# Kernel optimization log

Hardware: AMD Instinct MI355X
Metric: run time of the kernel (lower is better)

The kernel has to match this reference:

```python
import jax, jax.numpy as jnp
import numpy as np

MAX_ITER = 20
F_TOL = 1e-6
FREE_NUM = 64  # free_idx[1] + 1
TRUNC = (0, 512)  # truncate_idx


def setup_inputs() -> dict:
    key = jax.random.key(0)
    ks = jax.random.split(key, 8)
    bsz, in_dim, hid, out_dim, m = 1024, 512, 1024, 256, 128
    return {
        "b_primal": jax.random.normal(ks[0], (bsz, in_dim), jnp.float32),
        "W0": jax.random.normal(ks[1], (hid, in_dim), jnp.float32) / np.sqrt(in_dim).astype(np.float32),
        "b0": jnp.zeros((hid,), jnp.float32),
        "W1": jax.random.normal(ks[2], (hid, hid), jnp.float32) / np.sqrt(hid).astype(np.float32),
        "b1": jnp.zeros((hid,), jnp.float32),
        "W2": jax.random.normal(ks[3], (out_dim, hid), jnp.float32) / np.sqrt(hid).astype(np.float32),
        "b2": jnp.zeros((out_dim,), jnp.float32),
        "A": jax.random.normal(ks[4], (m, out_dim), jnp.float32) * 0.1,
        "b_vec": jax.random.normal(ks[5], (m,), jnp.float32),
        # scaled so spectral norm < 1 -> contracting fixed-point iteration
        "WzProj": jax.random.normal(ks[6], (out_dim, out_dim), jnp.float32) * 0.03,
        "WbProj": jax.random.normal(ks[7], (out_dim, m), jnp.float32) * 0.1,
    }


def reference(b_primal, W0, b0, W1, b1, W2, b2, A, b_vec, WzProj, WbProj):
    # eval-mode forward of DualNN (report_projection=True)
    x = b_primal[:, TRUNC[0]:TRUNC[1]]
    h = jax.nn.relu(x @ W0.T + b0)
    h = jax.nn.relu(h @ W1.T + b1)
    out = h @ W2.T + b2                      # [bsz, output_dim]

    bias_proj = b_vec @ WbProj.T             # [output_dim]

    def cond(state):
        _, it, res = state
        return (it <= MAX_ITER) & (res > F_TOL)

    def body(state):
        z, it, _ = state
        z = bias_proj + z @ WzProj.T         # affine projection step
        u = z[:, :FREE_NUM]
        v = jax.nn.relu(z[:, FREE_NUM:])     # clamp non-free coordinates
        z = jnp.concatenate([u, v], axis=-1)
        res = jnp.max(jnp.abs(z @ A.T - b_vec))  # inf-norm equality residual
        return z, it + 1, res

    z_star, curr_iter, _ = jax.lax.while_loop(
        cond, body, (out, jnp.int32(1), jnp.float32(jnp.inf)))
    return (z_star, out, curr_iter)
```

## Files before the change

### kernel.cpp

```cpp
#include <hip/hip_runtime.h>

typedef __attribute__((ext_vector_type(8))) __bf16 bf16x8;
typedef __attribute__((ext_vector_type(4))) float f32x4;

#define MAX_ITER_N 20
#define F_TOL_F 1e-6f
#define FREE_NUM_N 64

#define BSZ 1024
#define IN_DIM 512
#define HID 1024
#define OUT_DIM 256
#define M_CON 128

#define WS_DONE  0
#define WS_RES   8
#define WS_BP    48
#define WS_H1    304
#define WS_H2    (WS_H1 + 524288)
#define WS_W2C   (WS_H2 + 524288)
#define WS_WZG   (WS_W2C + 131072)
#define WS_AG    (WS_WZG + 32768)

__device__ __forceinline__ unsigned short f2bf(float f) {
    unsigned int u = __float_as_uint(f);
    u += 0x7fffu + ((u >> 16) & 1u);
    return (unsigned short)(u >> 16);
}

__device__ __forceinline__ unsigned int pk2(float a, float b) {
    return (unsigned int)f2bf(a) | ((unsigned int)f2bf(b) << 16);
}

__device__ __forceinline__ void cvt16(const float* s, unsigned short* d) {
    float4 v0 = *(const float4*)s,       v1 = *(const float4*)(s + 4),
           v2 = *(const float4*)(s + 8), v3 = *(const float4*)(s + 12);
    *(uint4*)d       = (uint4){pk2(v0.x, v0.y), pk2(v0.z, v0.w), pk2(v1.x, v1.y), pk2(v1.z, v1.w)};
    *(uint4*)(d + 8) = (uint4){pk2(v2.x, v2.y), pk2(v2.z, v2.w), pk2(v3.x, v3.y), pk2(v3.z, v3.w)};
}

__device__ __forceinline__ void gload_lds16(const unsigned short* g, unsigned short* l) {
    __builtin_amdgcn_global_load_lds(
        (const __attribute__((address_space(1))) unsigned int*)(const void*)g,
        (__attribute__((address_space(3))) unsigned int*)(void*)l, 16, 0, 0);
}

__device__ __forceinline__ bf16x8 frag128(const unsigned short* lds, int row, int gc) {
    int phys = gc ^ (row & 15);
    return __builtin_bit_cast(bf16x8, *(const uint4*)(lds + row * 128 + phys * 8));
}

template<int K, bool AF32, bool RELU>
__global__ __launch_bounds__(256) void gemm_k(
    const void* __restrict__ Ap, const float* __restrict__ Bf,
    const float* __restrict__ bias, unsigned short* __restrict__ C,
    float* __restrict__ ws,
    const float* __restrict__ W2, const float* __restrict__ Wz,
    const float* __restrict__ Am, const float* __restrict__ b_vec,
    const float* __restrict__ WbP)
{
    constexpr int NCH = K / 128;
    __shared__ __align__(16) unsigned short sA[2][8192];
    __shared__ __align__(16) unsigned short sB[2][8192];

    const int tid = threadIdx.x;

    if constexpr (AF32) {
        if (blockIdx.x >= 256) {
            int eb = blockIdx.x - 256;
            unsigned short* W2c = (unsigned short*)(ws + WS_W2C);
            unsigned short* WzG = (unsigned short*)(ws + WS_WZG);
            unsigned short* AG  = (unsigned short*)(ws + WS_AG);
            float* bp = ws + WS_BP;
            if (eb < 64) {
                int base = eb * 4096 + tid * 16;
                cvt16(W2 + base, W2c + base);
            } else if (eb < 80) {
                int base = (eb - 64) * 4096 + tid * 16;
                cvt16(Wz + base, WzG + base);
            } else if (eb < 88) {
                int base = (eb - 80) * 4096 + tid * 16;
                cvt16(Am + base, AG + base);
            } else {
                if (eb == 88 && tid < 48) ((unsigned int*)ws)[tid] = 0u;
                int j  = (eb - 88) * 32 + (tid >> 3);
                int kg = tid & 7;
                const float* p = WbP + j * M_CON + kg * 16;
                float s = 0.0f;
#pragma unroll
                for (int i = 0; i < 16; ++i) s += p[i] * b_vec[kg * 16 + i];
#pragma unroll
                for (int off = 4; off > 0; off >>= 1) s += __shfl_xor(s, off);
                if (kg == 0) bp[j] = s;
            }
            return;
        }
    }

    const int w = tid >> 6;
    const int lane = tid & 63;
    const int ln = lane & 15;
    const int q  = lane >> 4;
    const int wr = w >> 1;
    const int wc = w & 1;
    const int row0 = (blockIdx.x >> 4) * 64;
    const int col0 = (blockIdx.x & 15) * 64;

    int grow[4], ggc[4], lof[4];
#pragma unroll
    for (int i = 0; i < 4; ++i) {
        int P = tid + 256 * i;
        grow[i] = P >> 4; ggc[i] = P & 15;
        lof[i] = grow[i] * 128 + (ggc[i] ^ (grow[i] & 15)) * 8;
    }
    int soff[4], dbase[4];
    const unsigned short* Ab_h = (const unsigned short*)Ap + row0 * K;
    const float*          Ab_f = (const float*)Ap + row0 * K;
    if constexpr (!AF32) {
#pragma unroll
        for (int i = 0; i < 4; ++i) {
            int P = w * 256 + i * 64 + lane;
            int row = P >> 4, pgc = P & 15;
            soff[i]  = row * K + (pgc ^ (row & 15)) * 8;
            dbase[i] = (w * 256 + i * 64) * 8;
        }
    }
    const float* Bb = Bf + col0 * K;

    float4 ra[8], rb[8];

    if constexpr (AF32) {
#pragma unroll
        for (int i = 0; i < 4; ++i) {
            const float* s = Ab_f + grow[i] * K + ggc[i] * 8;
            ra[2*i]   = *(const float4*)s;
            ra[2*i+1] = *(const float4*)(s + 4);
        }
    } else {
#pragma unroll
        for (int i = 0; i < 4; ++i) gload_lds16(Ab_h + soff[i], &sA[0][dbase[i]]);
    }
#pragma unroll
    for (int i = 0; i < 4; ++i) {
        const float* s = Bb + grow[i] * K + ggc[i] * 8;
        rb[2*i]   = *(const float4*)s;
        rb[2*i+1] = *(const float4*)(s + 4);
    }
    if constexpr (AF32) {
#pragma unroll
        for (int i = 0; i < 4; ++i)
            *(uint4*)(&sA[0][lof[i]]) = (uint4){
                pk2(ra[2*i].x, ra[2*i].y),   pk2(ra[2*i].z, ra[2*i].w),
                pk2(ra[2*i+1].x, ra[2*i+1].y), pk2(ra[2*i+1].z, ra[2*i+1].w)};
    }
#pragma unroll
    for (int i = 0; i < 4; ++i)
        *(uint4*)(&sB[0][lof[i]]) = (uint4){
            pk2(rb[2*i].x, rb[2*i].y),   pk2(rb[2*i].z, rb[2*i].w),
            pk2(rb[2*i+1].x, rb[2*i+1].y), pk2(rb[2*i+1].z, rb[2*i+1].w)};

    f32x4 acc[2][2];
#pragma unroll
    for (int rm = 0; rm < 2; ++rm)
#pragma unroll
        for (int cn = 0; cn < 2; ++cn)
            acc[rm][cn] = (f32x4){0.f, 0.f, 0.f, 0.f};

    for (int c = 0; c < NCH; ++c) {
        __syncthreads();
        const int nb = (c + 1) & 1;
        if (c + 1 < NCH) {
            const int koff = (c + 1) * 128;
            if constexpr (AF32) {
#pragma unroll
                for (int i = 0; i < 4; ++i) {
                    const float* s = Ab_f + grow[i] * K + koff + ggc[i] * 8;
                    ra[2*i]   = *(const float4*)s;
                    ra[2*i+1] = *(const float4*)(s + 4);
                }
            } else {
#pragma unroll
                for (int i = 0; i < 4; ++i)
                    gload_lds16(Ab_h + koff + soff[i], &sA[nb][dbase[i]]);
            }
#pragma unroll
            for (int i = 0; i < 4; ++i) {
                const float* s = Bb + grow[i] * K + koff + ggc[i] * 8;
                rb[2*i]   = *(const float4*)s;
                rb[2*i+1] = *(const float4*)(s + 4);
            }
        }
        const unsigned short* Ac = sA[c & 1];
        const unsigned short* Bc = sB[c & 1];
#pragma unroll
        for (int ks = 0; ks < 4; ++ks) {
            bf16x8 af0 = frag128(Ac, wr * 32 + ln,      ks * 4 + q);
            bf16x8 af1 = frag128(Ac, wr * 32 + 16 + ln, ks * 4 + q);
            bf16x8 bf0 = frag128(Bc, wc * 32 + ln,      ks * 4 + q);
            bf16x8 bf1 = frag128(Bc, wc * 32 + 16 + ln, ks * 4 + q);
            acc[0][0] = __builtin_amdgcn_mfma_f32_16x16x32_bf16(af0, bf0, acc[0][0], 0, 0, 0);
            acc[0][1] = __builtin_amdgcn_mfma_f32_16x16x32_bf16(af0, bf1, acc[0][1], 0, 0, 0);
            acc[1][0] = __builtin_amdgcn_mfma_f32_16x16x32_bf16(af1, bf0, acc[1][0], 0, 0, 0);
            acc[1][1] = __builtin_amdgcn_mfma_f32_16x16x32_bf16(af1, bf1, acc[1][1], 0, 0, 0);
        }
        if (c + 1 < NCH) {
            if constexpr (AF32) {
#pragma unroll
                for (int i = 0; i < 4; ++i)
                    *(uint4*)(&sA[nb][lof[i]]) = (uint4){
                        pk2(ra[2*i].x, ra[2*i].y),   pk2(ra[2*i].z, ra[2*i].w),
                        pk2(ra[2*i+1].x, ra[2*i+1].y), pk2(ra[2*i+1].z, ra[2*i+1].w)};
            }
#pragma unroll
            for (int i = 0; i < 4; ++i)
                *(uint4*)(&sB[nb][lof[i]]) = (uint4){
                    pk2(rb[2*i].x, rb[2*i].y),   pk2(rb[2*i].z, rb[2*i].w),
                    pk2(rb[2*i+1].x, rb[2*i+1].y), pk2(rb[2*i+1].z, rb[2*i+1].w)};
        }
    }

#pragma unroll
    for (int cn = 0; cn < 2; ++cn) {
        const int cc = col0 + wc * 32 + cn * 16 + ln;
        const float bv = bias[cc];
#pragma unroll
        for (int rm = 0; rm < 2; ++rm)
#pragma unroll
            for (int i = 0; i < 4; ++i) {
                int r = row0 + wr * 32 + rm * 16 + q * 4 + i;
                float v = acc[rm][cn][i] + bv;
                if (RELU) v = fmaxf(v, 0.0f);
                C[r * HID + cc] = f2bf(v);
            }
    }
}

__global__ __launch_bounds__(512, 1) void k3_k(
    const float* __restrict__ b2v, const float* __restrict__ b_vec,
    const float* __restrict__ Wzf, float* __restrict__ out,
    float* __restrict__ ws)
{
    __shared__ __align__(16) unsigned short hS[16 * 1024];
    __shared__ __align__(16) unsigned short zS[2][16][264];
    __shared__ float redL[MAX_ITER_N * 8];
    __shared__ float Tsh;
    __shared__ int hotI;

    unsigned int* done = (unsigned int*)ws;
    unsigned int* res  = (unsigned int*)(ws + WS_RES);
    const float* bp = ws + WS_BP;
    const unsigned short* h2c = (const unsigned short*)(ws + WS_H2);
    const unsigned short* W2c = (const unsigned short*)(ws + WS_W2C);
    const unsigned short* WzG = (const unsigned short*)(ws + WS_WZG);
    const unsigned short* AG  = (const unsigned short*)(ws + WS_AG);
    float* outz = out + BSZ * OUT_DIM;

    const int tid  = threadIdx.x;
    const int wave = tid >> 6;
    const int lane = tid & 63;
    const int ln   = lane & 15;
    const int q    = lane >> 4;
    const int bid  = blockIdx.x;
    const int r0   = bid * 16;

#pragma unroll
    for (int i = 0; i < 4; ++i) {
        int G = wave * 256 + i * 64 + lane;
        int row = G >> 7, phys = G & 127;
        int gc = (phys & ~15) | ((phys & 15) ^ (row & 15));
        gload_lds16(h2c + (r0 + row) * HID + gc * 8, &hS[(wave * 256 + i * 64) * 8]);
    }

    int colg[2];
    colg[0] = wave * 32 + ln;
    colg[1] = wave * 32 + 16 + ln;
    const bool relu0 = (wave * 32) >= FREE_NUM_N;
    const bool relu1 = (wave * 32 + 16) >= FREE_NUM_N;

    bf16x8 afr[8];
    const int m = wave * 16 + ln;
    const float bvv = b_vec[m];
#pragma unroll
    for (int ks = 0; ks < 8; ++ks)
        afr[ks] = __builtin_bit_cast(bf16x8, *(const uint4*)(AG + m * OUT_DIM + ks * 32 + q * 8));
    float bpv[2];
    bf16x8 wzfr[2][8];
#pragma unroll
    for (int nt = 0; nt < 2; ++nt) {
        bpv[nt] = bp[colg[nt]];
#pragma unroll
        for (int ks = 0; ks < 8; ++ks)
            wzfr[nt][ks] = __builtin_bit_cast(bf16x8, *(const uint4*)(WzG + colg[nt] * OUT_DIM + ks * 32 + q * 8));
    }
    __syncthreads();

    const f32x4 zero4 = {0.f, 0.f, 0.f, 0.f};

    f32x4 a3a[2], a3b[2];
    a3a[0] = zero4; a3a[1] = zero4; a3b[0] = zero4; a3b[1] = zero4;
#pragma unroll 4
    for (int ks = 0; ks < 16; ++ks) {
        int gciA = ks * 4 + q;
        int physA = (gciA & ~15) | ((gciA & 15) ^ ln);
        bf16x8 afA = __builtin_bit_cast(bf16x8, *(const uint4*)&hS[ln * 1024 + physA * 8]);
        int gciB = (ks + 16) * 4 + q;
        int physB = (gciB & ~15) | ((gciB & 15) ^ ln);
        bf16x8 afB = __builtin_bit_cast(bf16x8, *(const uint4*)&hS[ln * 1024 + physB * 8]);
#pragma unroll
        for (int nt = 0; nt < 2; ++nt) {
            bf16x8 wfA = __builtin_bit_cast(bf16x8, *(const uint4*)(W2c + colg[nt] * HID + ks * 32 + q * 8));
            bf16x8 wfB = __builtin_bit_cast(bf16x8, *(const uint4*)(W2c + colg[nt] * HID + (ks + 16) * 32 + q * 8));
            a3a[nt] = __builtin_amdgcn_mfma_f32_16x16x32_bf16(afA, wfA, a3a[nt], 0, 0, 0);
            a3b[nt] = __builtin_amdgcn_mfma_f32_16x16x32_bf16(afB, wfB, a3b[nt], 0, 0, 0);
        }
    }

#pragma unroll
    for (int nt = 0; nt < 2; ++nt) {
        float bv = b2v[colg[nt]];
#pragma unroll
        for (int i = 0; i < 4; ++i) {
            float v = a3a[nt][i] + a3b[nt][i] + bv;
            outz[(r0 + q * 4 + i) * OUT_DIM + colg[nt]] = v;
            zS[0][q * 4 + i][colg[nt]] = f2bf(v);
        }
    }
    __syncthreads();

    bf16x8 zfr[8];
#pragma unroll
    for (int ks = 0; ks < 8; ++ks)
        zfr[ks] = __builtin_bit_cast(bf16x8, *(const uint4*)&zS[0][ln][ks * 32 + q * 8]);

    int wb = 1;

    for (int t = 1; t <= MAX_ITER_N; ++t) {
        f32x4 aA[2], aB[2], r2a, r2b;
        aA[0] = zero4; aA[1] = zero4; aB[0] = zero4; aB[1] = zero4;
        r2a = zero4; r2b = zero4;
#pragma unroll
        for (int ks = 0; ks < 4; ++ks) {
#pragma unroll
            for (int nt = 0; nt < 2; ++nt) {
                aA[nt] = __builtin_amdgcn_mfma_f32_16x16x32_bf16(zfr[ks],     wzfr[nt][ks],     aA[nt], 0, 0, 0);
                aB[nt] = __builtin_amdgcn_mfma_f32_16x16x32_bf16(zfr[ks + 4], wzfr[nt][ks + 4], aB[nt], 0, 0, 0);
            }
            if (t > 1) {
                r2a = __builtin_amdgcn_mfma_f32_16x16x32_bf16(zfr[ks],     afr[ks],     r2a, 0, 0, 0);
                r2b = __builtin_amdgcn_mfma_f32_16x16x32_bf16(zfr[ks + 4], afr[ks + 4], r2b, 0, 0, 0);
            }
        }
        float vals[2][4];
#pragma unroll
        for (int nt = 0; nt < 2; ++nt) {
            const bool rl = nt ? relu1 : relu0;
#pragma unroll
            for (int i = 0; i < 4; ++i) {
                float v = aA[nt][i] + aB[nt][i] + bpv[nt];
                if (rl) v = fmaxf(v, 0.0f);
                vals[nt][i] = v;
            }
        }
        if (t > 1) {
            float lmax = 0.0f;
#pragma unroll
            for (int i = 0; i < 4; ++i)
                lmax = fmaxf(lmax, fabsf(r2a[i] + r2b[i] - bvv));
#pragma unroll
            for (int off = 32; off > 0; off >>= 1)
                lmax = fmaxf(lmax, __shfl_xor(lmax, off));
            if (lane == 0) redL[(t - 2) * 8 + wave] = lmax;
        }
        if (t == MAX_ITER_N) {
#pragma unroll
            for (int nt = 0; nt < 2; ++nt)
#pragma unroll
                for (int i = 0; i < 4; ++i)
                    out[(r0 + q * 4 + i) * OUT_DIM + colg[nt]] = vals[nt][i];
        }
#pragma unroll
        for (int nt = 0; nt < 2; ++nt)
#pragma unroll
            for (int i = 0; i < 4; ++i)
                zS[wb][q * 4 + i][colg[nt]] = f2bf(vals[nt][i]);
        __syncthreads();
#pragma unroll
        for (int ks = 0; ks < 8; ++ks)
            zfr[ks] = __builtin_bit_cast(bf16x8, *(const uint4*)&zS[wb][ln][ks * 32 + q * 8]);
        wb ^= 1;
    }

    {
        f32x4 r2a = zero4, r2b = zero4;
#pragma unroll
        for (int ks = 0; ks < 4; ++ks) {
            r2a = __builtin_amdgcn_mfma_f32_16x16x32_bf16(zfr[ks],     afr[ks],     r2a, 0, 0, 0);
            r2b = __builtin_amdgcn_mfma_f32_16x16x32_bf16(zfr[ks + 4], afr[ks + 4], r2b, 0, 0, 0);
        }
        float lmax = 0.0f;
#pragma unroll
        for (int i = 0; i < 4; ++i)
            lmax = fmaxf(lmax, fabsf(r2a[i] + r2b[i] - bvv));
#pragma unroll
        for (int off = 32; off > 0; off >>= 1)
            lmax = fmaxf(lmax, __shfl_xor(lmax, off));
        if (lane == 0) redL[19 * 8 + wave] = lmax;
    }
    __syncthreads();

    bool lhot = true;
    if (tid < MAX_ITER_N) {
        float rv = redL[tid * 8];
#pragma unroll
        for (int w2 = 1; w2 < 8; ++w2) rv = fmaxf(rv, redL[tid * 8 + w2]);
        atomicMax(res + tid, __float_as_uint(rv));
        lhot = (rv > F_TOL_F);
    }
    if (tid < 64) {
        unsigned long long mm = __ballot((tid < MAX_ITER_N) && lhot);
        if (tid == 0) hotI = ((mm & 0xFFFFFull) == 0xFFFFFull) ? 1 : 0;
    }
    __syncthreads();

    if (tid == 0) {
        __threadfence();
        atomicAdd(done, 1u);
    }

    if (hotI) {
        if (bid == 0 && tid == 0)
            out[2 * BSZ * OUT_DIM] = (float)(MAX_ITER_N + 1);
        return;
    }

    if (tid == 0) {
        while (__hip_atomic_load(done, __ATOMIC_ACQUIRE, __HIP_MEMORY_SCOPE_AGENT) < 64u)
            __builtin_amdgcn_s_sleep(2);
    }
    __syncthreads();

    {
        float rv = 1e30f;
        if (tid < MAX_ITER_N)
            rv = __uint_as_float(__hip_atomic_load(res + tid, __ATOMIC_ACQUIRE, __HIP_MEMORY_SCOPE_AGENT));
        if (tid < 64) {
            unsigned long long mm = __ballot((tid < MAX_ITER_N) && !(rv > F_TOL_F));
            if (tid == 0) Tsh = (float)(mm ? (int)__ffsll(mm) : MAX_ITER_N);
        }
        __syncthreads();
    }
    const int T = (int)Tsh;
    if (bid == 0 && tid == 0)
        out[2 * BSZ * OUT_DIM] = (float)(T + 1);
    if (T >= MAX_ITER_N) return;

    {
        float (*zF)[257] = (float(*)[257])hS;
        const int row = tid >> 4;
        const int c0 = (tid & 15) * 16;
        if (tid < 256)
            for (int i = 0; i < 16; ++i)
                zF[row][c0 + i] = outz[(r0 + row) * OUT_DIM + c0 + i];
        __syncthreads();
        const int j = tid;
        const float bj = (tid < 256) ? bp[j] : 0.0f;
        for (int t = 0; t < T; ++t) {
            float acc[16] = {};
            if (tid < 256) {
                for (int k = 0; k < OUT_DIM; ++k) {
                    float wv = Wzf[j * OUT_DIM + k];
#pragma unroll
                    for (int r = 0; r < 16; ++r) acc[r] += zF[r][k] * wv;
                }
            }
            __syncthreads();
            if (tid < 256) {
#pragma unroll
                for (int r = 0; r < 16; ++r) {
                    float v = acc[r] + bj;
                    if (j >= FREE_NUM_N) v = fmaxf(v, 0.0f);
                    zF[r][j] = v;
                }
            }
            __syncthreads();
        }
        if (tid < 256)
            for (int i = 0; i < 16; ++i)
                out[(r0 + row) * OUT_DIM + c0 + i] = zF[row][c0 + i];
    }
}

extern "C" void kernel_launch(void* const* d_in, const int* in_sizes, int n_in,
                              void* d_out, int out_size, void* d_ws, size_t ws_size,
                              hipStream_t stream) {
    const float* b_primal = (const float*)d_in[0];
    const float* W0     = (const float*)d_in[1];
    const float* b0     = (const float*)d_in[2];
    const float* W1     = (const float*)d_in[3];
    const float* b1     = (const float*)d_in[4];
    const float* W2     = (const float*)d_in[5];
    const float* b2     = (const float*)d_in[6];
    const float* Amat   = (const float*)d_in[7];
    const float* b_vec  = (const float*)d_in[8];
    const float* WzProj = (const float*)d_in[9];
    const float* WbProj = (const float*)d_in[10];
    float* out = (float*)d_out;
    float* ws  = (float*)d_ws;

    unsigned short* h1c = (unsigned short*)(ws + WS_H1);
    unsigned short* h2c = (unsigned short*)(ws + WS_H2);

    hipLaunchKernelGGL((gemm_k<IN_DIM, true, true>), dim3(352), dim3(256), 0, stream,
                       (const void*)b_primal, W0, b0, h1c, ws,
                       W2, WzProj, Amat, b_vec, WbProj);
    hipLaunchKernelGGL((gemm_k<HID, false, true>), dim3(256), dim3(256), 0, stream,
                       (const void*)h1c, W1, b1, h2c, ws,
                       nullptr, nullptr, nullptr, nullptr, nullptr);
    hipLaunchKernelGGL(k3_k, dim3(64), dim3(512), 0, stream,
                       b2, b_vec, WzProj, out, ws);
}
```

Before: 137.6 us.

## Fuse second hidden-layer GEMM into fixed-point kernel and drop separate launch

Removes the standalone layer-2 GEMM launch and computes relu(h1 @ W1.T + b1) per 16-row block inside the final kernel, writing the result into a new swizzled LDS buffer that feeds the W2 GEMM. W1 is converted to bf16 by extra blocks in the first kernel, reusing the old h2 workspace region. This saves a launch and the h2 global round trip, but runs the largest GEMM on only 64 blocks, each streaming all of W1 from global memory, which risks lower parallelism and higher L2 traffic.

```diff
diff --git a/kernel.cpp b/kernel.cpp
--- a/kernel.cpp
+++ b/kernel.cpp
@@ -57,7 +57,7 @@
     float* __restrict__ ws,
     const float* __restrict__ W2, const float* __restrict__ Wz,
     const float* __restrict__ Am, const float* __restrict__ b_vec,
-    const float* __restrict__ WbP)
+    const float* __restrict__ WbP, const float* __restrict__ W1f)
 {
     constexpr int NCH = K / 128;
     __shared__ __align__(16) unsigned short sA[2][8192];
@@ -71,6 +71,7 @@
             unsigned short* W2c = (unsigned short*)(ws + WS_W2C);
             unsigned short* WzG = (unsigned short*)(ws + WS_WZG);
             unsigned short* AG  = (unsigned short*)(ws + WS_AG);
+            unsigned short* W1c = (unsigned short*)(ws + WS_H2);
             float* bp = ws + WS_BP;
             if (eb < 64) {
                 int base = eb * 4096 + tid * 16;
@@ -81,7 +82,7 @@
             } else if (eb < 88) {
                 int base = (eb - 80) * 4096 + tid * 16;
                 cvt16(Am + base, AG + base);
-            } else {
+            } else if (eb < 96) {
                 if (eb == 88 && tid < 48) ((unsigned int*)ws)[tid] = 0u;
                 int j  = (eb - 88) * 32 + (tid >> 3);
                 int kg = tid & 7;
@@ -92,6 +93,9 @@
 #pragma unroll
                 for (int off = 4; off > 0; off >>= 1) s += __shfl_xor(s, off);
                 if (kg == 0) bp[j] = s;
+            } else {
+                int base = (eb - 96) * 4096 + tid * 16;
+                cvt16(W1f + base, W1c + base);
             }
             return;
         }
@@ -236,11 +240,12 @@
 }
 
 __global__ __launch_bounds__(512, 1) void k3_k(
-    const float* __restrict__ b2v, const float* __restrict__ b_vec,
-    const float* __restrict__ Wzf, float* __restrict__ out,
-    float* __restrict__ ws)
+    const float* __restrict__ b1f, const float* __restrict__ b2v,
+    const float* __restrict__ b_vec, const float* __restrict__ Wzf,
+    float* __restrict__ out, float* __restrict__ ws)
 {
-    __shared__ __align__(16) unsigned short hS[16 * 1024];
+    __shared__ __align__(16) unsigned short hS1[16 * 1024];
+    __shared__ __align__(16) unsigned short hS2[16 * 1024];
     __shared__ __align__(16) unsigned short zS[2][16][264];
     __shared__ float redL[MAX_ITER_N * 8];
     __shared__ float Tsh;
@@ -249,7 +254,8 @@
     unsigned int* done = (unsigned int*)ws;
     unsigned int* res  = (unsigned int*)(ws + WS_RES);
     const float* bp = ws + WS_BP;
-    const unsigned short* h2c = (const unsigned short*)(ws + WS_H2);
+    const unsigned short* h1c = (const unsigned short*)(ws + WS_H1);
+    const unsigned short* W1c = (const unsigned short*)(ws + WS_H2);
     const unsigned short* W2c = (const unsigned short*)(ws + WS_W2C);
     const unsigned short* WzG = (const unsigned short*)(ws + WS_WZG);
     const unsigned short* AG  = (const unsigned short*)(ws + WS_AG);
@@ -268,7 +274,7 @@
         int G = wave * 256 + i * 64 + lane;
         int row = G >> 7, phys = G & 127;
         int gc = (phys & ~15) | ((phys & 15) ^ (row & 15));
-        gload_lds16(h2c + (r0 + row) * HID + gc * 8, &hS[(wave * 256 + i * 64) * 8]);
+        gload_lds16(h1c + (r0 + row) * HID + gc * 8, &hS1[(wave * 256 + i * 64) * 8]);
     }
 
     int colg[2];
@@ -292,9 +298,43 @@
         for (int ks = 0; ks < 8; ++ks)
             wzfr[nt][ks] = __builtin_bit_cast(bf16x8, *(const uint4*)(WzG + colg[nt] * OUT_DIM + ks * 32 + q * 8));
     }
+    float b1t[8];
+#pragma unroll
+    for (int ct = 0; ct < 8; ++ct) b1t[ct] = b1f[wave * 128 + ct * 16 + ln];
     __syncthreads();
 
     const f32x4 zero4 = {0.f, 0.f, 0.f, 0.f};
+
+    {
+        f32x4 hacc[8];
+#pragma unroll
+        for (int ct = 0; ct < 8; ++ct) hacc[ct] = zero4;
+#pragma unroll 2
+        for (int ks = 0; ks < 32; ++ks) {
+            int gci = ks * 4 + q;
+            int phys = (gci & ~15) | ((gci & 15) ^ ln);
+            bf16x8 af = __builtin_bit_cast(bf16x8, *(const uint4*)&hS1[ln * 1024 + phys * 8]);
+#pragma unroll
+            for (int ct = 0; ct < 8; ++ct) {
+                bf16x8 wf = __builtin_bit_cast(bf16x8,
+                    *(const uint4*)(W1c + (wave * 128 + ct * 16 + ln) * HID + ks * 32 + q * 8));
+                hacc[ct] = __builtin_amdgcn_mfma_f32_16x16x32_bf16(af, wf, hacc[ct], 0, 0, 0);
+            }
+        }
+#pragma unroll
+        for (int ct = 0; ct < 8; ++ct) {
+            const int c = wave * 128 + ct * 16 + ln;
+            const int g = c >> 3;
+#pragma unroll
+            for (int i = 0; i < 4; ++i) {
+                float v = fmaxf(hacc[ct][i] + b1t[ct], 0.0f);
+                int row = q * 4 + i;
+                int pg = (g & ~15) | ((g & 15) ^ (row & 15));
+                hS2[row * 1024 + pg * 8 + (c & 7)] = f2bf(v);
+            }
+        }
+    }
+    __syncthreads();
 
     f32x4 a3a[2], a3b[2];
     a3a[0] = zero4; a3a[1] = zero4; a3b[0] = zero4; a3b[1] = zero4;
@@ -302,10 +342,10 @@
     for (int ks = 0; ks < 16; ++ks) {
         int gciA = ks * 4 + q;
         int physA = (gciA & ~15) | ((gciA & 15) ^ ln);
-        bf16x8 afA = __builtin_bit_cast(bf16x8, *(const uint4*)&hS[ln * 1024 + physA * 8]);
+        bf16x8 afA = __builtin_bit_cast(bf16x8, *(const uint4*)&hS2[ln * 1024 + physA * 8]);
         int gciB = (ks + 16) * 4 + q;
         int physB = (gciB & ~15) | ((gciB & 15) ^ ln);
-        bf16x8 afB = __builtin_bit_cast(bf16x8, *(const uint4*)&hS[ln * 1024 + physB * 8]);
+        bf16x8 afB = __builtin_bit_cast(bf16x8, *(const uint4*)&hS2[ln * 1024 + physB * 8]);
 #pragma unroll
         for (int nt = 0; nt < 2; ++nt) {
             bf16x8 wfA = __builtin_bit_cast(bf16x8, *(const uint4*)(W2c + colg[nt] * HID + ks * 32 + q * 8));
@@ -455,7 +495,7 @@
     if (T >= MAX_ITER_N) return;
 
     {
-        float (*zF)[257] = (float(*)[257])hS;
+        float (*zF)[257] = (float(*)[257])hS1;
         const int row = tid >> 4;
         const int c0 = (tid & 15) * 16;
         if (tid < 256)
@@ -508,14 +548,10 @@
     float* ws  = (float*)d_ws;
 
     unsigned short* h1c = (unsigned short*)(ws + WS_H1);
-    unsigned short* h2c = (unsigned short*)(ws + WS_H2);
-
-    hipLaunchKernelGGL((gemm_k<IN_DIM, true, true>), dim3(352), dim3(256), 0, stream,
+
+    hipLaunchKernelGGL((gemm_k<IN_DIM, true, true>), dim3(608), dim3(256), 0, stream,
                        (const void*)b_primal, W0, b0, h1c, ws,
-                       W2, WzProj, Amat, b_vec, WbProj);
-    hipLaunchKernelGGL((gemm_k<HID, false, true>), dim3(256), dim3(256), 0, stream,
-                       (const void*)h1c, W1, b1, h2c, ws,
-                       nullptr, nullptr, nullptr, nullptr, nullptr);
+                       W2, WzProj, Amat, b_vec, WbProj, W1);
     hipLaunchKernelGGL(k3_k, dim3(64), dim3(512), 0, stream,
-                       b2, b_vec, WzProj, out, ws);
-}
+                       b1, b2, b_vec, WzProj, out, ws);
+}
```

After: 182.9 us. +32.9%, slower.
